# Performance work log

Measured on AMD Instinct MI355X. Metric: run time of the kernel, lower is better.

Reference implementation:

```python
import jax, jax.numpy as jnp
import numpy as np

STD = 1.0  # components_std from cfg
LOG_2PI = float(np.log(2.0 * np.pi))


def setup_inputs() -> dict:
    key = jax.random.key(0)
    k1, k2, k3 = jax.random.split(key, 3)
    B, S, D, K = 256, 1024, 32, 512
    x = jax.random.normal(k1, (B, S, D), dtype=jnp.float32)
    logits = jax.random.normal(k2, (B, K), dtype=jnp.float32)
    # xavier_normal_ init on (K, D): std = sqrt(2 / (K + D))
    means = jax.random.normal(k3, (K, D), dtype=jnp.float32) * np.sqrt(2.0 / (K + D))
    return {"x": x, "logits": logits, "means": means}


def reference(x, logits, means):
    # x: [B, S, D], logits: [B, K], means: [K, D]
    D = x.shape[-1]
    log_mix = jax.nn.log_softmax(logits, axis=-1)  # [B, K] Categorical log-probs
    # squared distance ||x - mu||^2 via expansion (avoids [B,S,K,D] intermediate)
    x2 = jnp.sum(x * x, axis=-1)          # [B, S]
    m2 = jnp.sum(means * means, axis=-1)  # [K]
    xm = jnp.einsum('bsd,kd->bsk', x, means)  # [B, S, K]
    sq = x2[..., None] - 2.0 * xm + m2        # [B, S, K]
    inv_var = 1.0 / (STD * STD)
    log_norm = D * (jnp.log(jnp.float32(STD)) + 0.5 * LOG_2PI)
    comp_logpdf = -0.5 * inv_var * sq - log_norm  # [B, S, K] Independent-Normal logpdf
    # mixture log_prob = logsumexp over components; NLL = negative
    nll = -jax.nn.logsumexp(log_mix[:, None, :] + comp_logpdf, axis=-1)  # [B, S]
    return nll
```

## Files before the change

kernel.cpp:

```cpp
#include <hip/hip_runtime.h>
#include <math.h>

constexpr int Bc = 256, Sc = 1024, Dc = 32, Kc = 512;
constexpr int ST = 256;
constexpr float LOG2E    = 1.4426950408889634f;
constexpr float LN2      = 0.6931471805599453f;
constexpr float LOG_NORM = 29.40603306051f;

typedef __attribute__((ext_vector_type(8))) short          bf16x8;
typedef __attribute__((ext_vector_type(8))) unsigned short u16x8;
typedef __attribute__((ext_vector_type(4))) unsigned short u16x4;
typedef __attribute__((ext_vector_type(4))) float          f32x4;

#if __has_builtin(__builtin_amdgcn_exp2f)
#define EXP2F(v) __builtin_amdgcn_exp2f(v)
#else
#define EXP2F(v) exp2f(v)
#endif
#if __has_builtin(__builtin_amdgcn_logf)
#define LOG2F(v) __builtin_amdgcn_logf(v)
#else
#define LOG2F(v) log2f(v)
#endif

__device__ __forceinline__ unsigned short f2bf(float f) {
    unsigned u = __float_as_uint(f);
    u += 0x7fff + ((u >> 16) & 1);
    return (unsigned short)(u >> 16);
}

__device__ __forceinline__ int swz(int row, int chunk) {
    return row * 32 + ((chunk ^ ((row >> 1) & 3)) << 3);
}

__global__ __launch_bounds__(256)
void gm_prep(const float* __restrict__ logits, const float* __restrict__ means,
             float* __restrict__ wbuf, unsigned short* __restrict__ mbf)
{
    __shared__ float csum[4096];
    __shared__ float red[8];
    const int tid  = threadIdx.x;
    const int lane = tid & 63;
    const int wid  = tid >> 6;
    const int b    = blockIdx.x;

    const float4* m4 = (const float4*)means;
    #pragma unroll
    for (int j = 0; j < 16; ++j) {
        const int i = tid + j * 256;
        float4 v = m4[i];
        csum[i] = v.x*v.x + v.y*v.y + v.z*v.z + v.w*v.w;
        if (b == 0) {
            u16x4 pk;
            pk[0] = f2bf(v.x); pk[1] = f2bf(v.y); pk[2] = f2bf(v.z); pk[3] = f2bf(v.w);
            *(u16x4*)&mbf[i * 4] = pk;
        }
    }

    const float l0 = logits[b * Kc + tid];
    const float l1 = logits[b * Kc + tid + 256];
    float mx = fmaxf(l0, l1);
    #pragma unroll
    for (int off = 32; off >= 1; off >>= 1) mx = fmaxf(mx, __shfl_xor(mx, off));
    if (lane == 0) red[wid] = mx;
    __syncthreads();
    mx = fmaxf(fmaxf(red[0], red[1]), fmaxf(red[2], red[3]));
    float sm = EXP2F((l0 - mx) * LOG2E) + EXP2F((l1 - mx) * LOG2E);
    #pragma unroll
    for (int off = 32; off >= 1; off >>= 1) sm += __shfl_xor(sm, off);
    if (lane == 0) red[4 + wid] = sm;
    __syncthreads();
    sm = red[4] + red[5] + red[6] + red[7];
    const float lse = mx + LN2 * LOG2F(sm);

    #pragma unroll
    for (int rr = 0; rr < 2; ++rr) {
        const int k = tid + rr * 256;
        const float* cs = &csum[k * 8];
        float m2 = ((cs[0] + cs[1]) + (cs[2] + cs[3]))
                 + ((cs[4] + cs[5]) + (cs[6] + cs[7]));
        const float lg = (rr == 0) ? l0 : l1;
        wbuf[(size_t)b * Kc + k] = EXP2F((lg - lse - 0.5f * m2) * LOG2E);
    }
}

__global__ __launch_bounds__(256, 4)
void gm_main(const float* __restrict__ x, const float* __restrict__ wbuf,
             const unsigned short* __restrict__ mbf, float* __restrict__ out)
{
    __shared__ unsigned short mlds[Kc * 32];
    __shared__ float wlds[Kc];
    __shared__ float x2p[ST];

    const int tid  = threadIdx.x;
    const int lane = tid & 63;
    const int wid  = tid >> 6;
    const int b    = blockIdx.x >> 2;
    const int s0   = (blockIdx.x & 3) * ST;
    const int q    = lane >> 4;
    const int ln   = lane & 15;
    const int rw   = wid * 64;

    {
        const u16x8* src = (const u16x8*)mbf;
        #pragma unroll
        for (int j = 0; j < 8; ++j) {
            const int c = tid + j * 256;
            *(u16x8*)&mlds[swz(c >> 2, c & 3)] = src[c];
        }
        wlds[tid]       = wbuf[(size_t)b * Kc + tid];
        wlds[tid + 256] = wbuf[(size_t)b * Kc + tid + 256];
    }

    bf16x8 a[4];
    #pragma unroll
    for (int t = 0; t < 4; ++t) {
        const int row = rw + 16 * t + ln;
        const float4* xp = (const float4*)(x + ((size_t)b * Sc + s0 + row) * Dc) + q * 2;
        float4 v0 = xp[0], v1 = xp[1];
        a[t][0]=(short)f2bf(v0.x*LOG2E); a[t][1]=(short)f2bf(v0.y*LOG2E);
        a[t][2]=(short)f2bf(v0.z*LOG2E); a[t][3]=(short)f2bf(v0.w*LOG2E);
        a[t][4]=(short)f2bf(v1.x*LOG2E); a[t][5]=(short)f2bf(v1.y*LOG2E);
        a[t][6]=(short)f2bf(v1.z*LOG2E); a[t][7]=(short)f2bf(v1.w*LOG2E);
        float p = v0.x*v0.x + v0.y*v0.y + v0.z*v0.z + v0.w*v0.w
                + v1.x*v1.x + v1.y*v1.y + v1.z*v1.z + v1.w*v1.w;
        p += __shfl_xor(p, 16); p += __shfl_xor(p, 32);
        if (q == 0) x2p[row] = p;
    }
    __syncthreads();

    const f32x4 zero = {0.f, 0.f, 0.f, 0.f};
    float acc[4][4] = {};

    #pragma unroll 4
    for (int kt = 0; kt < 32; ++kt) {
        const int krow = kt * 16 + ln;
        const bf16x8 bfr = *(const bf16x8*)&mlds[swz(krow, q)];
        const float  wv  = wlds[krow];
        f32x4 d0 = __builtin_amdgcn_mfma_f32_16x16x32_bf16(a[0], bfr, zero, 0, 0, 0);
        f32x4 d1 = __builtin_amdgcn_mfma_f32_16x16x32_bf16(a[1], bfr, zero, 0, 0, 0);
        f32x4 d2 = __builtin_amdgcn_mfma_f32_16x16x32_bf16(a[2], bfr, zero, 0, 0, 0);
        f32x4 d3 = __builtin_amdgcn_mfma_f32_16x16x32_bf16(a[3], bfr, zero, 0, 0, 0);
        #pragma unroll
        for (int r = 0; r < 4; ++r) {
            acc[0][r] = fmaf(wv, EXP2F(d0[r]), acc[0][r]);
            acc[1][r] = fmaf(wv, EXP2F(d1[r]), acc[1][r]);
            acc[2][r] = fmaf(wv, EXP2F(d2[r]), acc[2][r]);
            acc[3][r] = fmaf(wv, EXP2F(d3[r]), acc[3][r]);
        }
    }

    #pragma unroll
    for (int t = 0; t < 4; ++t) {
        #pragma unroll
        for (int r = 0; r < 4; ++r) {
            float v = acc[t][r];
            v += __shfl_xor(v, 1); v += __shfl_xor(v, 2);
            v += __shfl_xor(v, 4); v += __shfl_xor(v, 8);
            if (ln == 0) {
                const int row = rw + 16 * t + q * 4 + r;
                out[(size_t)b * Sc + s0 + row] =
                    0.5f * x2p[row] + LOG_NORM - LN2 * LOG2F(v);
            }
        }
    }
}

extern "C" void kernel_launch(void* const* d_in, const int* in_sizes, int n_in,
                              void* d_out, int out_size, void* d_ws, size_t ws_size,
                              hipStream_t stream) {
    const float* x      = (const float*)d_in[0];
    const float* logits = (const float*)d_in[1];
    const float* means  = (const float*)d_in[2];
    float* out = (float*)d_out;
    (void)in_sizes; (void)n_in; (void)out_size; (void)ws_size;

    unsigned short* mbf  = (unsigned short*)d_ws;
    float*          wbuf = (float*)((char*)d_ws + 32768);

    hipLaunchKernelGGL(gm_prep, dim3(Bc), dim3(256), 0, stream,
                       logits, means, wbuf, mbf);
    hipLaunchKernelGGL(gm_main, dim3(Bc * (Sc / ST)), dim3(256), 0, stream,
                       x, wbuf, mbf, out);
}
```

Before: 97.26 us.

## Fuse prep into main kernel and switch matmul to FP8 MFMA

Removes the separate prep kernel: each block now computes mean norms, the per-batch log-softmax and the mixture weights itself, and converts means to FP8 in shared memory. Both x and means are packed to FP8 and multiplied with the 16x16x32 fp8 MFMA instead of bf16, which halves LDS and register footprint for the operands. The log-sum-exp of the logits is folded in as an additive constant at the end. In exchange every block redundantly reads and converts all means, and FP8 quantisation of x*log2e inside an exponent risks large accuracy loss.

```diff
diff --git a/kernel.cpp b/kernel.cpp
--- a/kernel.cpp
+++ b/kernel.cpp
@@ -7,10 +7,7 @@
 constexpr float LN2      = 0.6931471805599453f;
 constexpr float LOG_NORM = 29.40603306051f;
 
-typedef __attribute__((ext_vector_type(8))) short          bf16x8;
-typedef __attribute__((ext_vector_type(8))) unsigned short u16x8;
-typedef __attribute__((ext_vector_type(4))) unsigned short u16x4;
-typedef __attribute__((ext_vector_type(4))) float          f32x4;
+typedef __attribute__((ext_vector_type(4))) float f32x4;
 
 #if __has_builtin(__builtin_amdgcn_exp2f)
 #define EXP2F(v) __builtin_amdgcn_exp2f(v)
@@ -23,74 +20,23 @@
 #define LOG2F(v) log2f(v)
 #endif
 
-__device__ __forceinline__ unsigned short f2bf(float f) {
-    unsigned u = __float_as_uint(f);
-    u += 0x7fff + ((u >> 16) & 1);
-    return (unsigned short)(u >> 16);
+template <bool HI>
+__device__ __forceinline__ int pkfp8(float a, float b, int old) {
+    return __builtin_amdgcn_cvt_pk_fp8_f32(a, b, old, HI);
 }
 
-__device__ __forceinline__ int swz(int row, int chunk) {
-    return row * 32 + ((chunk ^ ((row >> 1) & 3)) << 3);
-}
-
-__global__ __launch_bounds__(256)
-void gm_prep(const float* __restrict__ logits, const float* __restrict__ means,
-             float* __restrict__ wbuf, unsigned short* __restrict__ mbf)
-{
-    __shared__ float csum[4096];
-    __shared__ float red[8];
-    const int tid  = threadIdx.x;
-    const int lane = tid & 63;
-    const int wid  = tid >> 6;
-    const int b    = blockIdx.x;
-
-    const float4* m4 = (const float4*)means;
-    #pragma unroll
-    for (int j = 0; j < 16; ++j) {
-        const int i = tid + j * 256;
-        float4 v = m4[i];
-        csum[i] = v.x*v.x + v.y*v.y + v.z*v.z + v.w*v.w;
-        if (b == 0) {
-            u16x4 pk;
-            pk[0] = f2bf(v.x); pk[1] = f2bf(v.y); pk[2] = f2bf(v.z); pk[3] = f2bf(v.w);
-            *(u16x4*)&mbf[i * 4] = pk;
-        }
-    }
-
-    const float l0 = logits[b * Kc + tid];
-    const float l1 = logits[b * Kc + tid + 256];
-    float mx = fmaxf(l0, l1);
-    #pragma unroll
-    for (int off = 32; off >= 1; off >>= 1) mx = fmaxf(mx, __shfl_xor(mx, off));
-    if (lane == 0) red[wid] = mx;
-    __syncthreads();
-    mx = fmaxf(fmaxf(red[0], red[1]), fmaxf(red[2], red[3]));
-    float sm = EXP2F((l0 - mx) * LOG2E) + EXP2F((l1 - mx) * LOG2E);
-    #pragma unroll
-    for (int off = 32; off >= 1; off >>= 1) sm += __shfl_xor(sm, off);
-    if (lane == 0) red[4 + wid] = sm;
-    __syncthreads();
-    sm = red[4] + red[5] + red[6] + red[7];
-    const float lse = mx + LN2 * LOG2F(sm);
-
-    #pragma unroll
-    for (int rr = 0; rr < 2; ++rr) {
-        const int k = tid + rr * 256;
-        const float* cs = &csum[k * 8];
-        float m2 = ((cs[0] + cs[1]) + (cs[2] + cs[3]))
-                 + ((cs[4] + cs[5]) + (cs[6] + cs[7]));
-        const float lg = (rr == 0) ? l0 : l1;
-        wbuf[(size_t)b * Kc + k] = EXP2F((lg - lse - 0.5f * m2) * LOG2E);
-    }
+__device__ __forceinline__ int swz8(int row, int chunk) {
+    return row * 32 + ((chunk ^ ((row >> 2) & 3)) << 3);
 }
 
 __global__ __launch_bounds__(256, 4)
-void gm_main(const float* __restrict__ x, const float* __restrict__ wbuf,
-             const unsigned short* __restrict__ mbf, float* __restrict__ out)
+void gm_all(const float* __restrict__ x, const float* __restrict__ logits,
+            const float* __restrict__ means, float* __restrict__ out)
 {
-    __shared__ unsigned short mlds[Kc * 32];
+    __shared__ unsigned char mlds[Kc * 32];
     __shared__ float wlds[Kc];
     __shared__ float x2p[ST];
+    __shared__ float red[8];
 
     const int tid  = threadIdx.x;
     const int lane = tid & 63;
@@ -101,27 +47,44 @@
     const int ln   = lane & 15;
     const int rw   = wid * 64;
 
-    {
-        const u16x8* src = (const u16x8*)mbf;
+    float l0, l1;
+    #pragma unroll
+    for (int rr = 0; rr < 2; ++rr) {
+        const int row = tid + rr * 256;
+        const float4* mp = (const float4*)(means + (size_t)row * Dc);
+        float m2 = 0.f;
         #pragma unroll
-        for (int j = 0; j < 8; ++j) {
-            const int c = tid + j * 256;
-            *(u16x8*)&mlds[swz(c >> 2, c & 3)] = src[c];
+        for (int c = 0; c < 4; ++c) {
+            float4 va = mp[2 * c], vb = mp[2 * c + 1];
+            m2 += va.x*va.x + va.y*va.y + va.z*va.z + va.w*va.w
+                + vb.x*vb.x + vb.y*vb.y + vb.z*vb.z + vb.w*vb.w;
+            int2 pk;
+            pk.x = pkfp8<false>(va.x, va.y, 0);
+            pk.x = pkfp8<true >(va.z, va.w, pk.x);
+            pk.y = pkfp8<false>(vb.x, vb.y, 0);
+            pk.y = pkfp8<true >(vb.z, vb.w, pk.y);
+            *(int2*)&mlds[swz8(row, c)] = pk;
         }
-        wlds[tid]       = wbuf[(size_t)b * Kc + tid];
-        wlds[tid + 256] = wbuf[(size_t)b * Kc + tid + 256];
+        const float lg = logits[b * Kc + row];
+        if (rr == 0) l0 = lg; else l1 = lg;
+        wlds[row] = EXP2F((lg - 0.5f * m2) * LOG2E);
     }
 
-    bf16x8 a[4];
+    float mx = fmaxf(l0, l1);
+    #pragma unroll
+    for (int off = 32; off >= 1; off >>= 1) mx = fmaxf(mx, __shfl_xor(mx, off));
+    if (lane == 0) red[wid] = mx;
+
+    int2 A[4];
     #pragma unroll
     for (int t = 0; t < 4; ++t) {
         const int row = rw + 16 * t + ln;
         const float4* xp = (const float4*)(x + ((size_t)b * Sc + s0 + row) * Dc) + q * 2;
         float4 v0 = xp[0], v1 = xp[1];
-        a[t][0]=(short)f2bf(v0.x*LOG2E); a[t][1]=(short)f2bf(v0.y*LOG2E);
-        a[t][2]=(short)f2bf(v0.z*LOG2E); a[t][3]=(short)f2bf(v0.w*LOG2E);
-        a[t][4]=(short)f2bf(v1.x*LOG2E); a[t][5]=(short)f2bf(v1.y*LOG2E);
-        a[t][6]=(short)f2bf(v1.z*LOG2E); a[t][7]=(short)f2bf(v1.w*LOG2E);
+        A[t].x = pkfp8<false>(v0.x * LOG2E, v0.y * LOG2E, 0);
+        A[t].x = pkfp8<true >(v0.z * LOG2E, v0.w * LOG2E, A[t].x);
+        A[t].y = pkfp8<false>(v1.x * LOG2E, v1.y * LOG2E, 0);
+        A[t].y = pkfp8<true >(v1.z * LOG2E, v1.w * LOG2E, A[t].y);
         float p = v0.x*v0.x + v0.y*v0.y + v0.z*v0.z + v0.w*v0.w
                 + v1.x*v1.x + v1.y*v1.y + v1.z*v1.z + v1.w*v1.w;
         p += __shfl_xor(p, 16); p += __shfl_xor(p, 32);
@@ -129,18 +92,28 @@
     }
     __syncthreads();
 
+    const float mxb = fmaxf(fmaxf(red[0], red[1]), fmaxf(red[2], red[3]));
+    float sm = EXP2F((l0 - mxb) * LOG2E) + EXP2F((l1 - mxb) * LOG2E);
+    #pragma unroll
+    for (int off = 32; off >= 1; off >>= 1) sm += __shfl_xor(sm, off);
+    if (lane == 0) red[4 + wid] = sm;
+
     const f32x4 zero = {0.f, 0.f, 0.f, 0.f};
+    const long a0 = *(const long*)&A[0];
+    const long a1 = *(const long*)&A[1];
+    const long a2 = *(const long*)&A[2];
+    const long a3 = *(const long*)&A[3];
     float acc[4][4] = {};
 
-    #pragma unroll 4
+    #pragma unroll 2
     for (int kt = 0; kt < 32; ++kt) {
         const int krow = kt * 16 + ln;
-        const bf16x8 bfr = *(const bf16x8*)&mlds[swz(krow, q)];
-        const float  wv  = wlds[krow];
-        f32x4 d0 = __builtin_amdgcn_mfma_f32_16x16x32_bf16(a[0], bfr, zero, 0, 0, 0);
-        f32x4 d1 = __builtin_amdgcn_mfma_f32_16x16x32_bf16(a[1], bfr, zero, 0, 0, 0);
-        f32x4 d2 = __builtin_amdgcn_mfma_f32_16x16x32_bf16(a[2], bfr, zero, 0, 0, 0);
-        f32x4 d3 = __builtin_amdgcn_mfma_f32_16x16x32_bf16(a[3], bfr, zero, 0, 0, 0);
+        const long  bfr = *(const long*)&mlds[swz8(krow, q)];
+        const float wv  = wlds[krow];
+        f32x4 d0 = __builtin_amdgcn_mfma_f32_16x16x32_fp8_fp8(a0, bfr, zero, 0, 0, 0);
+        f32x4 d1 = __builtin_amdgcn_mfma_f32_16x16x32_fp8_fp8(a1, bfr, zero, 0, 0, 0);
+        f32x4 d2 = __builtin_amdgcn_mfma_f32_16x16x32_fp8_fp8(a2, bfr, zero, 0, 0, 0);
+        f32x4 d3 = __builtin_amdgcn_mfma_f32_16x16x32_fp8_fp8(a3, bfr, zero, 0, 0, 0);
         #pragma unroll
         for (int r = 0; r < 4; ++r) {
             acc[0][r] = fmaf(wv, EXP2F(d0[r]), acc[0][r]);
@@ -149,6 +122,9 @@
             acc[3][r] = fmaf(wv, EXP2F(d3[r]), acc[3][r]);
         }
     }
+    __syncthreads();
+    const float lse  = mxb + LN2 * LOG2F(red[4] + red[5] + red[6] + red[7]);
+    const float base = LOG_NORM + lse;
 
     #pragma unroll
     for (int t = 0; t < 4; ++t) {
@@ -160,7 +136,7 @@
             if (ln == 0) {
                 const int row = rw + 16 * t + q * 4 + r;
                 out[(size_t)b * Sc + s0 + row] =
-                    0.5f * x2p[row] + LOG_NORM - LN2 * LOG2F(v);
+                    0.5f * x2p[row] + base - LN2 * LOG2F(v);
             }
         }
     }
@@ -173,13 +149,8 @@
     const float* logits = (const float*)d_in[1];
     const float* means  = (const float*)d_in[2];
     float* out = (float*)d_out;
-    (void)in_sizes; (void)n_in; (void)out_size; (void)ws_size;
+    (void)in_sizes; (void)n_in; (void)out_size; (void)d_ws; (void)ws_size;
 
-    unsigned short* mbf  = (unsigned short*)d_ws;
-    float*          wbuf = (float*)((char*)d_ws + 32768);
-
-    hipLaunchKernelGGL(gm_prep, dim3(Bc), dim3(256), 0, stream,
-                       logits, means, wbuf, mbf);
-    hipLaunchKernelGGL(gm_main, dim3(Bc * (Sc / ST)), dim3(256), 0, stream,
-                       x, wbuf, mbf, out);
+    hipLaunchKernelGGL(gm_all, dim3(Bc * (Sc / ST)), dim3(256), 0, stream,
+                       x, logits, means, out);
 }
```

Measured after the change: 95.49 us. About the same (-1.8%).
